# Performance work log

Hardware: AMD Instinct MI355X
Metric: run time of the kernel (lower is better)

Reference implementation:

```python
import jax, jax.numpy as jnp
import numpy as np

D_IN, D_DICT, K, N = 768, 16384, 32, 8192


def setup_inputs() -> dict:
    key = jax.random.key(0)
    k1, k2, k3, k4, k5 = jax.random.split(key, 5)
    s_in = 1.0 / np.sqrt(D_IN)
    s_dict = 1.0 / np.sqrt(D_DICT)
    return {
        "x": jax.random.normal(k1, (N, D_IN), dtype=jnp.float32),
        # torch Linear: weight [out, in], bias [out]
        "W_enc": jax.random.uniform(k2, (D_DICT, D_IN), jnp.float32, -s_in, s_in),
        "b_enc": jax.random.uniform(k3, (D_DICT,), jnp.float32, -s_in, s_in),
        "W_dec": jax.random.uniform(k4, (D_IN, D_DICT), jnp.float32, -s_dict, s_dict),
        "b_dec": jax.random.uniform(k5, (D_IN,), jnp.float32, -s_dict, s_dict),
    }


def reference(x, W_enc, b_enc, W_dec, b_dec):
    # encode: z = x @ W_enc^T + b_enc  -> [N, d_dict]
    z = jnp.einsum("nd,kd->nk", x, W_enc) + b_enc
    # top-k mask along last dim (scatter 1.0 at top-k indices)
    _, idx = jax.lax.top_k(z, K)                      # idx: [N, K]
    rows = jnp.arange(z.shape[0])[:, None]            # [N, 1]
    mask = jnp.zeros_like(z).at[rows, idx].set(1.0)
    z_sparse = z * mask
    # decode: x_hat = z_sparse @ W_dec^T + b_dec -> [N, d_in]
    x_hat = jnp.einsum("nk,dk->nd", z_sparse, W_dec) + b_dec
    return (x_hat, z_sparse)
```

## Files before the change

kernel.cpp:

```cpp
#include <hip/hip_runtime.h>
#include <stdint.h>

#define D_IN   768
#define D_DICT 16384
#define NROWS  8192
#define TOPK   32
#define CAND_TARGET 40
#define CAND_MAX    80
#define FLOORU 0xBFA8u
#define NTILES 64
#define SEG    24
#define LECAP  768

#define BM 256
#define BN 256
#define BK 64
#define NKT (D_IN / BK)

typedef __attribute__((ext_vector_type(4))) float  f32x4;
typedef __attribute__((ext_vector_type(8))) short  s16x8;
typedef __attribute__((ext_vector_type(4))) unsigned short u16x4;

static __device__ __forceinline__ unsigned short f2bf(float f) {
    unsigned int u = __float_as_uint(f);
    unsigned int r = (u + 0x7FFFu + ((u >> 16) & 1u)) >> 16;
    return (unsigned short)r;
}
static __device__ __forceinline__ unsigned short bfmap(unsigned short u) {
    return (u & 0x8000u) ? (unsigned short)(~u) : (unsigned short)(u | 0x8000u);
}

static __device__ __forceinline__ void gload_lds16(const void* g, void* l) {
    __builtin_amdgcn_global_load_lds(
        (const __attribute__((address_space(1))) unsigned int*)g,
        (__attribute__((address_space(3))) unsigned int*)l, 16, 0, 0);
}

__global__ __launch_bounds__(256) void cast_bf16(const float4* __restrict__ in,
                                                 u16x4* __restrict__ out, int n4) {
    int idx = blockIdx.x * 256 + threadIdx.x;
    if (idx >= n4) return;
    float4 v = in[idx];
    u16x4 o;
    o.x = f2bf(v.x); o.y = f2bf(v.y); o.z = f2bf(v.z); o.w = f2bf(v.w);
    out[idx] = o;
}

__global__ void transpose_wdec(const float* __restrict__ in, float* __restrict__ out) {
    __shared__ float t[32][33];
    int bx = blockIdx.x, by = blockIdx.y;
    int tx = threadIdx.x, ty = threadIdx.y;
#pragma unroll
    for (int i = 0; i < 4; ++i)
        t[ty + i * 8][tx] = in[(size_t)(by * 32 + ty + i * 8) * D_DICT + bx * 32 + tx];
    __syncthreads();
#pragma unroll
    for (int i = 0; i < 4; ++i)
        out[(size_t)(bx * 32 + ty + i * 8) * D_IN + by * 32 + tx] = t[tx][ty + i * 8];
}

__global__ __launch_bounds__(512, 2) void gemm_enc(const unsigned short* __restrict__ Xb,
                                                   const unsigned short* __restrict__ Wb,
                                                   const float* __restrict__ bEnc,
                                                   unsigned int* __restrict__ list,
                                                   unsigned char* __restrict__ cnt8,
                                                   float* __restrict__ zsp) {
    extern __shared__ char smem[];
    unsigned short* As = (unsigned short*)smem;
    unsigned short* Bs = (unsigned short*)(smem + 65536);
    const int tid    = threadIdx.x;
    const int waveId = tid >> 6;
    const int lane   = tid & 63;

    const int wg    = blockIdx.x;
    const int wgid  = (wg & 7) * 256 + (wg >> 3);
    const int ctile = wgid & (NTILES - 1);
    const int rtile = wgid >> 6;
    const int rowBase = rtile * BM;
    const int colBase = ctile * BN;
    const int wm = waveId >> 2, wn = waveId & 3;

    f32x4 acc[8][4] = {};

    const int quad = lane >> 4;
    const int lr   = lane & 15;

    auto STAGEH = [&](int t, int kind, int kh) {
        const int d = t & 1;
        const unsigned short* gsrc = kind ? Wb : Xb;
        const int gbase = kind ? colBase : rowBase;
        unsigned short* lb = (kind ? Bs : As) + (size_t)(d * 2 + kh) * (256 * 32);
        const int k0 = t * BK + kh * 32;
#pragma unroll
        for (int i = 0; i < 2; ++i) {
            int slot = i * 512 + tid;
            int r = slot >> 2;
            int c = slot & 3;
            int lc = c ^ ((r >> 1) & 3);
            gload_lds16(gsrc + (size_t)(gbase + r) * D_IN + k0 + lc * 8,
                        lb + (size_t)(i * 512 + waveId * 64) * 8);
        }
    };

    STAGEH(0, 0, 0); STAGEH(0, 1, 0);
    STAGEH(0, 0, 1); STAGEH(0, 1, 1);
    STAGEH(1, 0, 0); STAGEH(1, 1, 0);

    for (int t = 0; t < NKT; ++t) {
        const int d = t & 1;
#pragma unroll
        for (int ph = 0; ph < 4; ++ph) {
            const int kh = ph >> 1, mh = ph & 1;
            if (ph == 0) {
                if (t + 1 < NKT) asm volatile("s_waitcnt vmcnt(8)" ::: "memory");
                else             asm volatile("s_waitcnt vmcnt(4)" ::: "memory");
            } else if (ph == 2) {
                if (t + 1 < NKT) asm volatile("s_waitcnt vmcnt(8)" ::: "memory");
                else             asm volatile("s_waitcnt vmcnt(0)" ::: "memory");
            }
            __builtin_amdgcn_s_barrier();

            const unsigned short* Ah = As + (size_t)(d * 2 + kh) * (256 * 32);
            const unsigned short* Bh = Bs + (size_t)(d * 2 + kh) * (256 * 32);
            s16x8 a[4], b[4];
#pragma unroll
            for (int j = 0; j < 4; ++j) {
                int ar = wm * 128 + (mh * 4 + j) * 16 + lr;
                a[j] = *(const s16x8*)(Ah + ar * 32 + ((quad ^ ((ar >> 1) & 3)) << 3));
            }
#pragma unroll
            for (int j = 0; j < 4; ++j) {
                int br = wn * 64 + j * 16 + lr;
                b[j] = *(const s16x8*)(Bh + br * 32 + ((quad ^ ((br >> 1) & 3)) << 3));
            }

            if      (ph == 0) { if (t + 1 < NKT) STAGEH(t + 1, 0, 1); }
            else if (ph == 1) { if (t + 1 < NKT) STAGEH(t + 1, 1, 1); }
            else if (ph == 2) { if (t + 2 < NKT) STAGEH(t + 2, 0, 0); }
            else              { if (t + 2 < NKT) STAGEH(t + 2, 1, 0); }

            __builtin_amdgcn_s_setprio(1);
#pragma unroll
            for (int j = 0; j < 4; ++j)
#pragma unroll
                for (int ni = 0; ni < 4; ++ni)
                    acc[mh * 4 + j][ni] = __builtin_amdgcn_mfma_f32_16x16x32_bf16(
                        a[j], b[ni], acc[mh * 4 + j][ni], 0, 0, 0);
            __builtin_amdgcn_s_setprio(0);
        }
    }

    int*          lcnt  = (int*)smem;
    unsigned int* stage = (unsigned int*)(smem + 1024);
    if (tid < 256) lcnt[tid] = 0;
    __syncthreads();

    {
        float4 z4 = make_float4(0.f, 0.f, 0.f, 0.f);
        float4* zd = (float4*)(zsp + (size_t)rowBase * D_DICT + colBase);
#pragma unroll
        for (int i = 0; i < 32; ++i) {
            int slot = i * 512 + tid;
            zd[(size_t)(slot >> 6) * (D_DICT / 4) + (slot & 63)] = z4;
        }
    }

    const int colW = colBase + wn * 64 + lr;
    float bias[4];
#pragma unroll
    for (int f = 0; f < 4; ++f) bias[f] = bEnc[colW + f * 16];
    const unsigned long long qmask = 0xFFFFull << (quad * 16);
    const unsigned long long lmask = (1ull << lane) - 1ull;

#pragma unroll
    for (int mi = 0; mi < 8; ++mi) {
#pragma unroll
        for (int rg = 0; rg < 4; ++rg) {
            const int lrow = wm * 128 + mi * 16 + quad * 4 + rg;
            unsigned int uv[4];
            unsigned long long bm[4];
            int m4 = 0;
#pragma unroll
            for (int f = 0; f < 4; ++f) {
                float v = acc[mi][f][rg] + bias[f];
                unsigned int u = bfmap(f2bf(v));
                uv[f] = (u << 16) | (unsigned int)(colW + f * 16);
                bool pass = (u >= FLOORU);
                bm[f] = __ballot(pass);
                if (pass) m4 |= (1 << f);
            }
            int rowTotal = (int)(__popcll(bm[0] & qmask) + __popcll(bm[1] & qmask)
                               + __popcll(bm[2] & qmask) + __popcll(bm[3] & qmask));
            int base = 0;
            if ((lane & 15) == 0 && rowTotal) base = atomicAdd(&lcnt[lrow], rowTotal);
            base = __shfl(base, quad * 16, 64);
            if (m4) {
                int pre = 0;
#pragma unroll
                for (int f = 0; f < 4; ++f) {
                    if (m4 & (1 << f)) {
                        int pos = base + pre + (int)__popcll(bm[f] & qmask & lmask);
                        if (pos < SEG) stage[lrow * SEG + pos] = uv[f];
                    }
                    pre += (int)__popcll(bm[f] & qmask);
                }
            }
        }
    }
    __syncthreads();

    if (tid < 256) {
        int c = lcnt[tid]; if (c > SEG) c = SEG;
        cnt8[(size_t)(rowBase + tid) * NTILES + ctile] = (unsigned char)c;
    }
    for (int i = tid; i < 256 * SEG; i += 512) {
        int r = i / SEG, s = i - r * SEG;
        int c = lcnt[r]; if (c > SEG) c = SEG;
        if (s < c)
            list[((size_t)(rowBase + r) * NTILES + ctile) * SEG + s] = stage[r * SEG + s];
    }
}

__global__ __launch_bounds__(256) void sel_dec(const unsigned int* __restrict__ list,
                                               const unsigned char* __restrict__ cnt8,
                                               const float* __restrict__ x,
                                               const float* __restrict__ wEnc,
                                               const float* __restrict__ bEnc,
                                               const float* __restrict__ wDecT,
                                               const float* __restrict__ bDec,
                                               float* __restrict__ zsp,
                                               float* __restrict__ xhat) {
    const int row = blockIdx.x;
    const int tid = threadIdx.x;
    const int waveId = tid >> 6;

    __shared__ int   histc[4][256];
    alignas(16) __shared__ float xs[D_IN];
    __shared__ unsigned int le[LECAP];
    __shared__ unsigned int cw[NTILES / 4];
    __shared__ int   tb[NTILES];
    __shared__ int   cidx[CAND_MAX];
    __shared__ float zc[CAND_MAX];
    __shared__ int   selk[TOPK];
    __shared__ float selv[TOPK];
    __shared__ int   sh_ncand, sh_bin, sh_cum, sh_bin2;
    __shared__ int   sh_nstrict, sh_ntie, sh_nsel;

    if (tid < NTILES / 4)
        cw[tid] = ((const unsigned int*)(cnt8 + (size_t)row * NTILES))[tid];
    if (tid < 192)
        ((float4*)xs)[tid] = ((const float4*)(x + (size_t)row * D_IN))[tid];
    if (tid == 0) { sh_nstrict = 0; sh_ntie = 0; sh_nsel = 0; sh_bin = -1; }
    __syncthreads();

    const unsigned char* cb = (const unsigned char*)cw;
    if (tid < 64) {
        int c = cb[tid];
        int pref = c;
#pragma unroll
        for (int off = 1; off < 64; off <<= 1) {
            int n = __shfl_up(pref, off, 64);
            if (tid >= off) pref += n;
        }
        tb[tid] = pref - c;
        if (tid == 63) sh_ncand = pref;
    }
    for (int b = tid; b < 1024; b += 256) ((int*)histc)[b] = 0;
    __syncthreads();
    const int nCand = min(sh_ncand, LECAP);

    for (int i = tid; i < NTILES * SEG; i += 256) {
        int t = i / SEG, s = i - t * SEG;
        if (s < (int)cb[t]) {
            int dst = tb[t] + s;
            if (dst < LECAP) le[dst] = list[((size_t)row * NTILES + t) * SEG + s];
        }
    }
    __syncthreads();

    const int T = CAND_TARGET;
    for (int i = tid; i < nCand; i += 256) {
        unsigned int u = le[i] >> 16;
        int bin = (int)((u - FLOORU) >> 6);
        if (bin > 255) bin = 255;
        atomicAdd(&histc[waveId][bin], 1);
    }
    __syncthreads();
    if (tid < 256) histc[0][tid] += histc[1][tid] + histc[2][tid] + histc[3][tid];
    __syncthreads();
    if (tid < 64) {
        int l = tid;
        int b0 = 255 - l * 4;
        int s0 = histc[0][b0], s1 = histc[0][b0 - 1],
            s2 = histc[0][b0 - 2], s3 = histc[0][b0 - 3];
        int local = s0 + s1 + s2 + s3;
        int pref = local;
#pragma unroll
        for (int off = 1; off < 64; off <<= 1) {
            int n = __shfl_up(pref, off, 64);
            if (l >= off) pref += n;
        }
        unsigned long long m = __ballot(pref >= T);
        if (m) {
            int first = (int)__ffsll(m) - 1;
            if (l == first) {
                int cum = pref - local;
                int b, c;
                if      (cum + s0 >= T)           { b = b0;     c = cum; }
                else if (cum + s0 + s1 >= T)      { b = b0 - 1; c = cum + s0; }
                else if (cum + s0 + s1 + s2 >= T) { b = b0 - 2; c = cum + s0 + s1; }
                else                              { b = b0 - 3; c = cum + s0 + s1 + s2; }
                sh_bin = b; sh_cum = c;
            }
        }
    }
    __syncthreads();
    const int b1 = sh_bin;
    unsigned int tieLo, tieTop;

    if (b1 >= 0) {
        const int cumAbove = sh_cum;
        for (int b = tid; b < 1024; b += 256) ((int*)histc)[b] = 0;
        __syncthreads();
        for (int i = tid; i < nCand; i += 256) {
            unsigned int u = le[i] >> 16;
            int bin = (int)((u - FLOORU) >> 6);
            if (bin > 255) bin = 255;
            if (bin == b1) atomicAdd(&histc[waveId][(u - FLOORU) & 63u], 1);
        }
        __syncthreads();
        if (tid < 64) {
            int l = tid;
            int bb = 63 - l;
            int local = histc[0][bb] + histc[1][bb] + histc[2][bb] + histc[3][bb];
            int pref = local;
#pragma unroll
            for (int off = 1; off < 64; off <<= 1) {
                int n = __shfl_up(pref, off, 64);
                if (l >= off) pref += n;
            }
            unsigned long long m = __ballot(cumAbove + pref >= T);
            int first = (int)__ffsll(m) - 1;
            if (l == first) sh_bin2 = bb;
        }
        __syncthreads();
        tieLo  = FLOORU + ((unsigned)b1 << 6) + (unsigned)sh_bin2;
        tieTop = tieLo;
    } else {
        tieLo = 1u; tieTop = 0u;
    }

    for (int i = tid; i < nCand; i += 256) {
        unsigned int u = le[i] >> 16;
        int col = (int)(le[i] & 0xFFFFu);
        if (u > tieTop) {
            int p = atomicAdd(&sh_nstrict, 1);
            cidx[p] = col;
        } else if (u >= tieLo) {
            int t = atomicAdd(&sh_ntie, 1);
            if (t < CAND_TARGET) cidx[CAND_MAX - 1 - t] = col;
        }
    }
    __syncthreads();
    const int nstrict = sh_nstrict;
    const int nt = min(sh_ntie, CAND_TARGET);
    int tmpv = 0;
    if (tid < nt) tmpv = cidx[CAND_MAX - 1 - tid];
    __syncthreads();
    if (tid < nt) cidx[nstrict + tid] = tmpv;
    __syncthreads();
    const int nc = nstrict + nt;

    const int sub = tid & 7;
    const int cq  = tid >> 3;
    for (int c0 = 0; c0 < nc; c0 += 32) {
        int c = c0 + cq;
        double a0 = 0.0, a1 = 0.0, a2 = 0.0, a3 = 0.0;
        int k = 0;
        if (c < nc) {
            k = cidx[c];
            const float4* wp = (const float4*)(wEnc + (size_t)k * D_IN);
            const float4* xp = (const float4*)xs;
#pragma unroll 8
            for (int j = 0; j < 24; ++j) {
                float4 wv = wp[j * 8 + sub];
                float4 xv = xp[j * 8 + sub];
                a0 += (double)xv.x * (double)wv.x;
                a1 += (double)xv.y * (double)wv.y;
                a2 += (double)xv.z * (double)wv.z;
                a3 += (double)xv.w * (double)wv.w;
            }
        }
        double acc = (a0 + a1) + (a2 + a3);
        acc += __shfl_xor(acc, 1, 64);
        acc += __shfl_xor(acc, 2, 64);
        acc += __shfl_xor(acc, 4, 64);
        if (c < nc && sub == 0) zc[c] = (float)(acc + (double)bEnc[k]);
    }
    __syncthreads();

    if (tid < nc) {
        float v = zc[tid];
        int   k = cidx[tid];
        int rk = 0;
        for (int j = 0; j < nc; ++j) {
            float vj = zc[j];
            if (vj > v || (vj == v && cidx[j] < k)) ++rk;
        }
        if (rk < TOPK) {
            int s = atomicAdd(&sh_nsel, 1);
            selk[s] = k; selv[s] = v;
        }
    }
    __syncthreads();

    if (tid < TOPK) zsp[(size_t)row * D_DICT + selk[tid]] = selv[tid];

    if (tid < 192) {
        float4 acc = ((const float4*)bDec)[tid];
#pragma unroll 8
        for (int j = 0; j < TOPK; ++j) {
            const float4* wr = (const float4*)(wDecT + (size_t)selk[j] * D_IN);
            float4 wv = wr[tid];
            float s = selv[j];
            acc.x += s * wv.x; acc.y += s * wv.y;
            acc.z += s * wv.z; acc.w += s * wv.w;
        }
        ((float4*)(xhat + (size_t)row * D_IN))[tid] = acc;
    }
}

extern "C" void kernel_launch(void* const* d_in, const int* in_sizes, int n_in,
                              void* d_out, int out_size, void* d_ws, size_t ws_size,
                              hipStream_t stream) {
    const float* x    = (const float*)d_in[0];
    const float* wEnc = (const float*)d_in[1];
    const float* bEnc = (const float*)d_in[2];
    const float* wDec = (const float*)d_in[3];
    const float* bDec = (const float*)d_in[4];

    float* xhat = (float*)d_out;
    float* zsp  = (float*)d_out + (size_t)NROWS * D_IN;

    char* ws = (char*)d_ws;
    unsigned short* Xb   = (unsigned short*)ws;
    unsigned short* Wb   = (unsigned short*)(ws + (size_t)NROWS * D_IN * 2);
    float*          WdT  = (float*)(ws + (size_t)NROWS * D_IN * 2
                                       + (size_t)D_DICT * D_IN * 2);
    unsigned int*   list = (unsigned int*)(ws + 88080384);
    unsigned char*  cnt8 = (unsigned char*)(ws + 88080384
                                       + (size_t)NROWS * NTILES * SEG * 4);

    static int configured = 0;
    if (!configured) {
        hipFuncSetAttribute((const void*)gemm_enc,
                            hipFuncAttributeMaxDynamicSharedMemorySize, 131072);
        configured = 1;
    }

    {
        int n4 = NROWS * D_IN / 4;
        cast_bf16<<<(n4 + 255) / 256, 256, 0, stream>>>((const float4*)x, (u16x4*)Xb, n4);
    }
    {
        int n4 = D_DICT * D_IN / 4;
        cast_bf16<<<(n4 + 255) / 256, 256, 0, stream>>>((const float4*)wEnc, (u16x4*)Wb, n4);
    }
    transpose_wdec<<<dim3(D_DICT / 32, D_IN / 32), dim3(32, 8), 0, stream>>>(wDec, WdT);
    gemm_enc<<<(NROWS / BM) * (D_DICT / BN), 512, 131072, stream>>>(Xb, Wb, bEnc, list, cnt8, zsp);
    sel_dec<<<NROWS, 256, 0, stream>>>(list, cnt8, x, wEnc, bEnc, WdT, bDec, zsp, xhat);
}
```

Measured before the change: 1.184 ms.

## Replace histogram threshold selection with rank sort, fuse casts, skip empty rows

The two-pass radix histogram that picked about 40 candidates per row is replaced by an O(n^2) rank computation in shared memory that keeps the top 64 candidates by bf16 key. The GEMM epilogue compares float values against a float floor and skips the atomic and staging work for row groups with no passing values. The two bf16 cast launches are merged into one kernel. Exact rescoring now runs on up to 64 candidates instead of about 40, and the quadratic rank loop can become costly when a row has many candidates.

```diff
diff --git a/kernel.cpp b/kernel.cpp
--- a/kernel.cpp
+++ b/kernel.cpp
@@ -5,9 +5,8 @@
 #define D_DICT 16384
 #define NROWS  8192
 #define TOPK   32
-#define CAND_TARGET 40
-#define CAND_MAX    80
-#define FLOORU 0xBFA8u
+#define CAND_TARGET 64
+#define FLOORF 1.30859375f
 #define NTILES 64
 #define SEG    24
 #define LECAP  768
@@ -36,14 +35,19 @@
         (__attribute__((address_space(3))) unsigned int*)l, 16, 0, 0);
 }
 
-__global__ __launch_bounds__(256) void cast_bf16(const float4* __restrict__ in,
-                                                 u16x4* __restrict__ out, int n4) {
+__global__ __launch_bounds__(256) void cast_both(const float4* __restrict__ inx,
+                                                 u16x4* __restrict__ outx, int n4x,
+                                                 const float4* __restrict__ inw,
+                                                 u16x4* __restrict__ outw, int n4w) {
     int idx = blockIdx.x * 256 + threadIdx.x;
-    if (idx >= n4) return;
-    float4 v = in[idx];
+    const float4* in; u16x4* out; int i;
+    if (idx < n4x) { in = inx; out = outx; i = idx; }
+    else if (idx < n4x + n4w) { in = inw; out = outw; i = idx - n4x; }
+    else return;
+    float4 v = in[i];
     u16x4 o;
     o.x = f2bf(v.x); o.y = f2bf(v.y); o.z = f2bf(v.z); o.w = f2bf(v.w);
-    out[idx] = o;
+    out[i] = o;
 }
 
 __global__ void transpose_wdec(const float* __restrict__ in, float* __restrict__ out) {
@@ -177,22 +181,22 @@
 #pragma unroll
         for (int rg = 0; rg < 4; ++rg) {
             const int lrow = wm * 128 + mi * 16 + quad * 4 + rg;
-            unsigned int uv[4];
+            float vv[4];
             unsigned long long bm[4];
             int m4 = 0;
 #pragma unroll
             for (int f = 0; f < 4; ++f) {
-                float v = acc[mi][f][rg] + bias[f];
-                unsigned int u = bfmap(f2bf(v));
-                uv[f] = (u << 16) | (unsigned int)(colW + f * 16);
-                bool pass = (u >= FLOORU);
+                vv[f] = acc[mi][f][rg] + bias[f];
+                bool pass = (vv[f] >= FLOORF);
                 bm[f] = __ballot(pass);
                 if (pass) m4 |= (1 << f);
             }
+            unsigned long long any = bm[0] | bm[1] | bm[2] | bm[3];
+            if (!(any & qmask)) continue;
             int rowTotal = (int)(__popcll(bm[0] & qmask) + __popcll(bm[1] & qmask)
                                + __popcll(bm[2] & qmask) + __popcll(bm[3] & qmask));
             int base = 0;
-            if ((lane & 15) == 0 && rowTotal) base = atomicAdd(&lcnt[lrow], rowTotal);
+            if ((lane & 15) == 0) base = atomicAdd(&lcnt[lrow], rowTotal);
             base = __shfl(base, quad * 16, 64);
             if (m4) {
                 int pre = 0;
@@ -200,7 +204,9 @@
                 for (int f = 0; f < 4; ++f) {
                     if (m4 & (1 << f)) {
                         int pos = base + pre + (int)__popcll(bm[f] & qmask & lmask);
-                        if (pos < SEG) stage[lrow * SEG + pos] = uv[f];
+                        unsigned int u = bfmap(f2bf(vv[f]));
+                        if (pos < SEG)
+                            stage[lrow * SEG + pos] = (u << 16) | (unsigned int)(colW + f * 16);
                     }
                     pre += (int)__popcll(bm[f] & qmask);
                 }
@@ -232,25 +238,22 @@
                                                float* __restrict__ xhat) {
     const int row = blockIdx.x;
     const int tid = threadIdx.x;
-    const int waveId = tid >> 6;
-
-    __shared__ int   histc[4][256];
+
     alignas(16) __shared__ float xs[D_IN];
     __shared__ unsigned int le[LECAP];
     __shared__ unsigned int cw[NTILES / 4];
     __shared__ int   tb[NTILES];
-    __shared__ int   cidx[CAND_MAX];
-    __shared__ float zc[CAND_MAX];
+    __shared__ int   cidx[CAND_TARGET];
+    __shared__ float zc[CAND_TARGET];
     __shared__ int   selk[TOPK];
     __shared__ float selv[TOPK];
-    __shared__ int   sh_ncand, sh_bin, sh_cum, sh_bin2;
-    __shared__ int   sh_nstrict, sh_ntie, sh_nsel;
+    __shared__ int   sh_ncand, sh_nsel;
 
     if (tid < NTILES / 4)
         cw[tid] = ((const unsigned int*)(cnt8 + (size_t)row * NTILES))[tid];
     if (tid < 192)
         ((float4*)xs)[tid] = ((const float4*)(x + (size_t)row * D_IN))[tid];
-    if (tid == 0) { sh_nstrict = 0; sh_ntie = 0; sh_nsel = 0; sh_bin = -1; }
+    if (tid == 0) sh_nsel = 0;
     __syncthreads();
 
     const unsigned char* cb = (const unsigned char*)cw;
@@ -265,7 +268,6 @@
         tb[tid] = pref - c;
         if (tid == 63) sh_ncand = pref;
     }
-    for (int b = tid; b < 1024; b += 256) ((int*)histc)[b] = 0;
     __syncthreads();
     const int nCand = min(sh_ncand, LECAP);
 
@@ -278,98 +280,15 @@
     }
     __syncthreads();
 
-    const int T = CAND_TARGET;
-    for (int i = tid; i < nCand; i += 256) {
-        unsigned int u = le[i] >> 16;
-        int bin = (int)((u - FLOORU) >> 6);
-        if (bin > 255) bin = 255;
-        atomicAdd(&histc[waveId][bin], 1);
-    }
-    __syncthreads();
-    if (tid < 256) histc[0][tid] += histc[1][tid] + histc[2][tid] + histc[3][tid];
-    __syncthreads();
-    if (tid < 64) {
-        int l = tid;
-        int b0 = 255 - l * 4;
-        int s0 = histc[0][b0], s1 = histc[0][b0 - 1],
-            s2 = histc[0][b0 - 2], s3 = histc[0][b0 - 3];
-        int local = s0 + s1 + s2 + s3;
-        int pref = local;
-#pragma unroll
-        for (int off = 1; off < 64; off <<= 1) {
-            int n = __shfl_up(pref, off, 64);
-            if (l >= off) pref += n;
-        }
-        unsigned long long m = __ballot(pref >= T);
-        if (m) {
-            int first = (int)__ffsll(m) - 1;
-            if (l == first) {
-                int cum = pref - local;
-                int b, c;
-                if      (cum + s0 >= T)           { b = b0;     c = cum; }
-                else if (cum + s0 + s1 >= T)      { b = b0 - 1; c = cum + s0; }
-                else if (cum + s0 + s1 + s2 >= T) { b = b0 - 2; c = cum + s0 + s1; }
-                else                              { b = b0 - 3; c = cum + s0 + s1 + s2; }
-                sh_bin = b; sh_cum = c;
-            }
-        }
-    }
-    __syncthreads();
-    const int b1 = sh_bin;
-    unsigned int tieLo, tieTop;
-
-    if (b1 >= 0) {
-        const int cumAbove = sh_cum;
-        for (int b = tid; b < 1024; b += 256) ((int*)histc)[b] = 0;
-        __syncthreads();
-        for (int i = tid; i < nCand; i += 256) {
-            unsigned int u = le[i] >> 16;
-            int bin = (int)((u - FLOORU) >> 6);
-            if (bin > 255) bin = 255;
-            if (bin == b1) atomicAdd(&histc[waveId][(u - FLOORU) & 63u], 1);
-        }
-        __syncthreads();
-        if (tid < 64) {
-            int l = tid;
-            int bb = 63 - l;
-            int local = histc[0][bb] + histc[1][bb] + histc[2][bb] + histc[3][bb];
-            int pref = local;
-#pragma unroll
-            for (int off = 1; off < 64; off <<= 1) {
-                int n = __shfl_up(pref, off, 64);
-                if (l >= off) pref += n;
-            }
-            unsigned long long m = __ballot(cumAbove + pref >= T);
-            int first = (int)__ffsll(m) - 1;
-            if (l == first) sh_bin2 = bb;
-        }
-        __syncthreads();
-        tieLo  = FLOORU + ((unsigned)b1 << 6) + (unsigned)sh_bin2;
-        tieTop = tieLo;
-    } else {
-        tieLo = 1u; tieTop = 0u;
-    }
-
-    for (int i = tid; i < nCand; i += 256) {
-        unsigned int u = le[i] >> 16;
-        int col = (int)(le[i] & 0xFFFFu);
-        if (u > tieTop) {
-            int p = atomicAdd(&sh_nstrict, 1);
-            cidx[p] = col;
-        } else if (u >= tieLo) {
-            int t = atomicAdd(&sh_ntie, 1);
-            if (t < CAND_TARGET) cidx[CAND_MAX - 1 - t] = col;
-        }
-    }
-    __syncthreads();
-    const int nstrict = sh_nstrict;
-    const int nt = min(sh_ntie, CAND_TARGET);
-    int tmpv = 0;
-    if (tid < nt) tmpv = cidx[CAND_MAX - 1 - tid];
-    __syncthreads();
-    if (tid < nt) cidx[nstrict + tid] = tmpv;
-    __syncthreads();
-    const int nc = nstrict + nt;
+    for (int c = tid; c < nCand; c += 256) {
+        unsigned int kc = le[c] ^ 0xFFFFu;
+        int rk = 0;
+        for (int j = 0; j < nCand; ++j)
+            rk += ((le[j] ^ 0xFFFFu) > kc) ? 1 : 0;
+        if (rk < CAND_TARGET) cidx[rk] = (int)(le[c] & 0xFFFFu);
+    }
+    __syncthreads();
+    const int nc = min(nCand, CAND_TARGET);
 
     const int sub = tid & 7;
     const int cq  = tid >> 3;
@@ -459,12 +378,10 @@
     }
 
     {
-        int n4 = NROWS * D_IN / 4;
-        cast_bf16<<<(n4 + 255) / 256, 256, 0, stream>>>((const float4*)x, (u16x4*)Xb, n4);
-    }
-    {
-        int n4 = D_DICT * D_IN / 4;
-        cast_bf16<<<(n4 + 255) / 256, 256, 0, stream>>>((const float4*)wEnc, (u16x4*)Wb, n4);
+        int n4x = NROWS * D_IN / 4;
+        int n4w = D_DICT * D_IN / 4;
+        cast_both<<<(n4x + n4w + 255) / 256, 256, 0, stream>>>(
+            (const float4*)x, (u16x4*)Xb, n4x, (const float4*)wEnc, (u16x4*)Wb, n4w);
     }
     transpose_wdec<<<dim3(D_DICT / 32, D_IN / 32), dim3(32, 8), 0, stream>>>(wDec, WdT);
     gemm_enc<<<(NROWS / BM) * (D_DICT / BN), 512, 131072, stream>>>(Xb, Wb, bEnc, list, cnt8, zsp);
```

Measured after the change: 1.247 ms. 5.3% more time.
